# Optimization experiments

Measured on AMD Instinct MI355X. Metric: run time of the kernel, lower is better.

The kernel has to match this reference:

```python
import jax, jax.numpy as jnp
import numpy as np

D_MODEL = 1024
N_HEADS = 16
SCALES = (1, 2)
D_K = D_MODEL // N_HEADS          # 64
HPS = N_HEADS // len(SCALES)      # heads per scale = 8


def _upsample_linear(x, target_len):
    """PyTorch F.interpolate(mode='linear', align_corners=False) along dim 2.
    x: [b, h, l, d] -> [b, h, target_len, d]"""
    b, h, l, d = x.shape
    if l == target_len:
        return x
    # source coordinates, clamped at 0 like PyTorch's area_pixel_compute_source_index
    coords = (jnp.arange(target_len, dtype=jnp.float32) + 0.5) * (l / target_len) - 0.5
    coords = jnp.maximum(coords, 0.0)
    i0 = jnp.clip(jnp.floor(coords).astype(jnp.int32), 0, l - 1)
    i1 = jnp.minimum(i0 + 1, l - 1)
    w = (coords - i0.astype(jnp.float32))[None, None, :, None]
    return x[:, :, i0, :] * (1.0 - w) + x[:, :, i1, :] * w


def setup_inputs() -> dict:
    rng = jax.random.key(0)
    ks = jax.random.split(rng, 7)
    B, S = 2, 2048
    s = 1.0 / np.sqrt(D_MODEL)
    mkw = lambda k: jax.random.normal(k, (D_MODEL, D_MODEL), jnp.float32) * s
    zb = jnp.zeros((D_MODEL,), jnp.float32)
    return {
        "query": jax.random.normal(ks[0], (B, S, D_MODEL), jnp.float32),
        "key": jax.random.normal(ks[1], (B, S, D_MODEL), jnp.float32),
        "value": jax.random.normal(ks[2], (B, S, D_MODEL), jnp.float32),
        "w_q": mkw(ks[3]), "b_q": zb,
        "w_k": mkw(ks[4]), "b_k": zb,
        "w_v": mkw(ks[5]), "b_v": zb,
        "w_o": mkw(ks[6]), "b_o": zb,
    }


def reference(query, key, value, w_q, b_q, w_k, b_k, w_v, b_v, w_o, b_o):
    B, S, _ = query.shape
    inv_scale = 1.0 / np.sqrt(D_K).astype(np.float32)

    def proj(x, W, b):
        # [B,S,D] -> [B,H,S,dk]
        return (x @ W + b).reshape(B, S, N_HEADS, D_K).transpose(0, 2, 1, 3)

    Q = proj(query, w_q, b_q)
    K = proj(key, w_k, b_k)
    V = proj(value, w_v, b_v)

    outs = []
    for i, f in enumerate(SCALES):
        hs = slice(i * HPS, (i + 1) * HPS)
        Qd = Q[:, hs, ::f]                      # strided downsample along seq
        Kd = K[:, hs, ::f]
        Vd = V[:, hs, ::f]
        scores = jnp.einsum('bhqd,bhkd->bhqk', Qd, Kd) * inv_scale
        attn = jax.nn.softmax(scores, axis=-1)   # dropout inactive (eval)
        o = jnp.einsum('bhqk,bhkd->bhqd', attn, Vd)
        outs.append(_upsample_linear(o, S))

    out = jnp.concatenate(outs, axis=1)          # [B,H,S,dk]
    out = out.transpose(0, 2, 1, 3).reshape(B, S, D_MODEL)
    return out @ w_o + b_o
```

## Files before the change

kernel.cpp:

```cpp
#include <hip/hip_runtime.h>
#include <hip/hip_bf16.h>
#include <cstddef>

#define DMODEL 1024
#define DK 64
#define S1 2048
#define S2 1024
#define NBATCH 2
#define NSPLIT 2
#define KVTILE 64

typedef __bf16 bf16x8 __attribute__((ext_vector_type(8)));
typedef float f32x4 __attribute__((ext_vector_type(4)));
typedef unsigned short u16x4 __attribute__((ext_vector_type(4)));
typedef unsigned int u32x4 __attribute__((ext_vector_type(4)));

__device__ __forceinline__ unsigned short f2bf(float f) {
  unsigned u = __builtin_bit_cast(unsigned, f);
  u = (u + 0x7FFFu + ((u >> 16) & 1u)) >> 16;
  return (unsigned short)u;
}
__device__ __forceinline__ float bf2f(unsigned short u) {
  unsigned x = ((unsigned)u) << 16;
  return __builtin_bit_cast(float, x);
}
__device__ __forceinline__ unsigned pack2bf(float a, float b) {
  return (unsigned)f2bf(a) | ((unsigned)f2bf(b) << 16);
}
__device__ __forceinline__ bf16x8 ld_bf16x8(const unsigned short* p) {
  u32x4 v = *reinterpret_cast<const u32x4*>(p);
  return __builtin_bit_cast(bf16x8, v);
}
__device__ __forceinline__ void gload_lds16(const void* g, void* l) {
  __builtin_amdgcn_global_load_lds(
      (const __attribute__((address_space(1))) unsigned*)g,
      (__attribute__((address_space(3))) unsigned*)l, 16, 0, 0);
}
__device__ __forceinline__ bf16x8 ld_tile(const unsigned short* tile, int row, int cbytes) {
  const char* p = (const char*)tile + row * 128 + (cbytes ^ ((row & 7) << 4));
  return ld_bf16x8((const unsigned short*)p);
}

__global__ __launch_bounds__(256) void cvt_bf16_kernel(
    const float* __restrict__ in, unsigned short* __restrict__ out, int n4) {
  int i = blockIdx.x * 256 + threadIdx.x;
  if (i >= n4) return;
  f32x4 v = reinterpret_cast<const f32x4*>(in)[i];
  u16x4 r;
#pragma unroll
  for (int j = 0; j < 4; ++j) r[j] = f2bf(v[j]);
  reinterpret_cast<u16x4*>(out)[i] = r;
}

__global__ __launch_bounds__(1024) void transpose_w_kernel(
    const float* __restrict__ W, unsigned short* __restrict__ Wt) {
  __shared__ float t[32][33];
  int tx = threadIdx.x, ty = threadIdx.y;
  int n = blockIdx.x * 32 + tx;
  int k = blockIdx.y * 32 + ty;
  t[ty][tx] = W[(size_t)k * DMODEL + n];
  __syncthreads();
  int n2 = blockIdx.x * 32 + ty;
  int k2 = blockIdx.y * 32 + tx;
  Wt[(size_t)n2 * DMODEL + k2] = f2bf(t[tx][ty]);
}

template <int MODE>
__global__ __launch_bounds__(256) void gemm_bf16(
    const unsigned short* __restrict__ A, const unsigned short* __restrict__ Bt,
    const float* __restrict__ bias, float* __restrict__ outF,
    unsigned short* __restrict__ out1, unsigned short* __restrict__ out2) {
  __shared__ __align__(16) unsigned short As[2][128 * 64];
  __shared__ __align__(16) unsigned short Bs[2][64 * 64];
  int w = threadIdx.x >> 6, lane = threadIdx.x & 63;
  int lo = lane & 15, hi = lane >> 4;
  int rowBase = blockIdx.y * 128;
  int colBase = blockIdx.x * 64;
  int rl = lane >> 3;
  int ck = lane & 7;

  auto stageA = [&](int buf, int k0) {
#pragma unroll
    for (int i = 0; i < 4; ++i) {
      int slot = w * 4 + i;
      int rloc = slot * 8 + rl;
      int cb = (ck * 16) ^ ((rloc & 7) << 4);
      const char* g = (const char*)(A + (size_t)(rowBase + rloc) * DMODEL + k0) + cb;
      gload_lds16(g, (void*)&As[buf][slot * 512]);
    }
  };
  auto stageB = [&](int buf, int k0) {
#pragma unroll
    for (int i = 0; i < 2; ++i) {
      int slot = w * 2 + i;
      int rloc = slot * 8 + rl;
      int cb = (ck * 16) ^ ((rloc & 7) << 4);
      const char* g = (const char*)(Bt + (size_t)(colBase + rloc) * DMODEL + k0) + cb;
      gload_lds16(g, (void*)&Bs[buf][slot * 512]);
    }
  };

  f32x4 acc[2][4] = {};

  stageA(0, 0);
  stageB(0, 0);
  __syncthreads();

  const int NT = DMODEL / 64;
  for (int t = 0; t < NT; ++t) {
    int buf = t & 1;
    if (t + 1 < NT) {
      stageA(buf ^ 1, (t + 1) * 64);
      stageB(buf ^ 1, (t + 1) * 64);
    }
    bf16x8 af[2][2], bfr[4][2];
#pragma unroll
    for (int mt = 0; mt < 2; ++mt)
#pragma unroll
      for (int kk = 0; kk < 2; ++kk)
        af[mt][kk] = ld_tile(&As[buf][0], w * 32 + mt * 16 + lo, kk * 64 + hi * 16);
#pragma unroll
    for (int nt = 0; nt < 4; ++nt)
#pragma unroll
      for (int kk = 0; kk < 2; ++kk)
        bfr[nt][kk] = ld_tile(&Bs[buf][0], nt * 16 + lo, kk * 64 + hi * 16);
#pragma unroll
    for (int kk = 0; kk < 2; ++kk)
#pragma unroll
      for (int mt = 0; mt < 2; ++mt)
#pragma unroll
        for (int nt = 0; nt < 4; ++nt)
          acc[mt][nt] = __builtin_amdgcn_mfma_f32_16x16x32_bf16(
              af[mt][kk], bfr[nt][kk], acc[mt][nt], 0, 0, 0);
    __syncthreads();
  }

#pragma unroll
  for (int mt = 0; mt < 2; ++mt) {
#pragma unroll
    for (int nt = 0; nt < 4; ++nt) {
      int col = colBase + nt * 16 + lo;
      float bv = bias[col];
#pragma unroll
      for (int r = 0; r < 4; ++r) {
        int row = rowBase + w * 32 + mt * 16 + hi * 4 + r;
        float v = acc[mt][nt][r] + bv;
        if (MODE == 0) {
          outF[(size_t)row * DMODEL + col] = v;
        } else {
          int b = row >> 11, s = row & 2047;
          int h = col >> 6, d = col & 63;
          if (MODE == 1) {
            if (h < 8)
              out1[(((size_t)(b * 8 + h)) * S1 + s) * DK + d] = f2bf(v);
            else if (!(s & 1))
              out2[(((size_t)(b * 8 + (h - 8))) * S2 + (s >> 1)) * DK + d] = f2bf(v);
          } else {
            if (h < 8)
              out1[(((size_t)(b * 8 + h)) * DK + d) * S1 + s] = f2bf(v);
            else if (!(s & 1))
              out2[(((size_t)(b * 8 + (h - 8))) * DK + d) * S2 + (s >> 1)] = f2bf(v);
          }
        }
      }
    }
  }
}

__global__ __launch_bounds__(256) void attn_kernel(
    const unsigned short* __restrict__ Q, const unsigned short* __restrict__ K,
    const unsigned short* __restrict__ Vt, float* __restrict__ Opart,
    float* __restrict__ ml, int Sq, int Skv) {
  __shared__ __align__(16) unsigned short KV[2][2][64 * 64];
  __shared__ __align__(16) unsigned P_lds[4][16][36];
  int w = threadIdx.x >> 6, lane = threadIdx.x & 63;
  int lo = lane & 15, hi = lane >> 4;
  int bh = blockIdx.z;
  int split = blockIdx.y;
  int q0 = blockIdx.x * 64 + w * 16;
  int splitLen = Skv / NSPLIT;
  int kvbase = split * splitLen;
  int nIter = splitLen / KVTILE;

  const unsigned short* Qp = Q + ((size_t)bh * Sq + q0) * DK;
  bf16x8 qb0 = ld_bf16x8(Qp + lo * DK + hi * 8);
  bf16x8 qb1 = ld_bf16x8(Qp + lo * DK + 32 + hi * 8);

  const unsigned short* Kb = K + (size_t)bh * Skv * DK;
  const unsigned short* Vb = Vt + (size_t)bh * DK * Skv;

  auto stage = [&](int buf, int kv0) {
    int rl = lane >> 3;
    int cbl = (lane & 7) * 16;
#pragma unroll
    for (int i = 0; i < 2; ++i) {
      int rt = w * 16 + i * 8 + rl;
      int gcb = cbl ^ ((rt & 7) << 4);
      const char* gK = (const char*)(Kb + (size_t)(kv0 + rt) * DK) + gcb;
      gload_lds16(gK, (void*)&KV[buf][0][(w * 16 + i * 8) * 64]);
      const char* gV = (const char*)(Vb + (size_t)rt * Skv + kv0) + gcb;
      gload_lds16(gV, (void*)&KV[buf][1][(w * 16 + i * 8) * 64]);
    }
  };

  float m = -1e30f, l = 0.f;
  f32x4 oacc[4] = {};

  stage(0, kvbase);
  __syncthreads();

  for (int it = 0; it < nIter; ++it) {
    if (it + 1 < nIter) stage((it + 1) & 1, kvbase + (it + 1) * KVTILE);

    const unsigned short* Kt = &KV[it & 1][0][0];
    const unsigned short* Vtl = &KV[it & 1][1][0];

    f32x4 s[4];
#pragma unroll
    for (int t = 0; t < 4; ++t) {
      bf16x8 ka0 = ld_tile(Kt, t * 16 + lo, hi * 16);
      bf16x8 ka1 = ld_tile(Kt, t * 16 + lo, 64 + hi * 16);
      f32x4 z = {};
      z = __builtin_amdgcn_mfma_f32_16x16x32_bf16(ka0, qb0, z, 0, 0, 0);
      s[t] = __builtin_amdgcn_mfma_f32_16x16x32_bf16(ka1, qb1, z, 0, 0, 0);
    }

    float x[16];
#pragma unroll
    for (int t = 0; t < 4; ++t)
#pragma unroll
      for (int r = 0; r < 4; ++r) x[t * 4 + r] = s[t][r] * 0.125f;
    float tmax = x[0];
#pragma unroll
    for (int j = 1; j < 16; ++j) tmax = fmaxf(tmax, x[j]);
    tmax = fmaxf(tmax, __shfl_xor(tmax, 16));
    tmax = fmaxf(tmax, __shfl_xor(tmax, 32));
    float mnew = fmaxf(m, tmax);
    float alpha = __expf(m - mnew);
    m = mnew;
    float tsum = 0.f;
#pragma unroll
    for (int j = 0; j < 16; ++j) {
      x[j] = __expf(x[j] - mnew);
      tsum += x[j];
    }
    tsum += __shfl_xor(tsum, 16);
    tsum += __shfl_xor(tsum, 32);
    l = l * alpha + tsum;

    unsigned* prow = &P_lds[w][lo][0];
#pragma unroll
    for (int t = 0; t < 4; ++t) {
      uint2 pk;
      pk.x = pack2bf(x[t * 4 + 0], x[t * 4 + 1]);
      pk.y = pack2bf(x[t * 4 + 2], x[t * 4 + 3]);
      *reinterpret_cast<uint2*>(prow + t * 8 + 2 * hi) = pk;
    }

    float ar[4];
#pragma unroll
    for (int r = 0; r < 4; ++r) ar[r] = __shfl(alpha, hi * 4 + r);
#pragma unroll
    for (int nb = 0; nb < 4; ++nb) {
      f32x4 t = oacc[nb];
      t[0] *= ar[0];
      t[1] *= ar[1];
      t[2] *= ar[2];
      t[3] *= ar[3];
      oacc[nb] = t;
    }

    bf16x8 pa0 = ld_bf16x8(reinterpret_cast<unsigned short*>(prow + 4 * hi));
    bf16x8 pa1 = ld_bf16x8(reinterpret_cast<unsigned short*>(prow + 16 + 4 * hi));
#pragma unroll
    for (int nb = 0; nb < 4; ++nb) {
      bf16x8 vb0 = ld_tile(Vtl, nb * 16 + lo, hi * 16);
      bf16x8 vb1 = ld_tile(Vtl, nb * 16 + lo, 64 + hi * 16);
      oacc[nb] = __builtin_amdgcn_mfma_f32_16x16x32_bf16(pa0, vb0, oacc[nb], 0, 0, 0);
      oacc[nb] = __builtin_amdgcn_mfma_f32_16x16x32_bf16(pa1, vb1, oacc[nb], 0, 0, 0);
    }

    __syncthreads();
  }

  float* Op = Opart + (((size_t)(split * 16 + bh)) * Sq + q0) * DK;
#pragma unroll
  for (int nb = 0; nb < 4; ++nb)
#pragma unroll
    for (int r = 0; r < 4; ++r)
      Op[(size_t)(hi * 4 + r) * DK + nb * 16 + lo] = oacc[nb][r];
  if (hi == 0) {
    float2* mlp = reinterpret_cast<float2*>(ml) + ((size_t)(split * 16 + bh)) * Sq + q0 + lo;
    *mlp = make_float2(m, l);
  }
}

template <int MODE>
__global__ __launch_bounds__(256) void combine_kernel(
    const float* __restrict__ Opart, const float* __restrict__ ml,
    unsigned short* __restrict__ out, int Sq) {
  int rr = blockIdx.x * 4 + (threadIdx.x >> 6);
  int d = threadIdx.x & 63;
  int bh = rr / Sq, q = rr - bh * Sq;
  const float2* mlp = reinterpret_cast<const float2*>(ml);
  float2 ml0 = mlp[(size_t)bh * Sq + q];
  float2 ml1 = mlp[(size_t)(16 + bh) * Sq + q];
  float M = fmaxf(ml0.x, ml1.x);
  float w0 = __expf(ml0.x - M), w1 = __expf(ml1.x - M);
  float inv = 1.0f / (ml0.y * w0 + ml1.y * w1);
  float o0 = Opart[((size_t)bh * Sq + q) * DK + d];
  float o1 = Opart[((size_t)(16 + bh) * Sq + q) * DK + d];
  float v = (o0 * w0 + o1 * w1) * inv;
  if (MODE == 1) {
    int b = bh >> 3, h = bh & 7;
    out[((size_t)(b * S1 + q)) * DMODEL + h * 64 + d] = f2bf(v);
  } else {
    out[((size_t)bh * Sq + q) * DK + d] = f2bf(v);
  }
}

__global__ __launch_bounds__(256) void upsample_kernel(
    const unsigned short* __restrict__ O2, unsigned short* __restrict__ ctx) {
  int c = blockIdx.x * 256 + threadIdx.x;
  if (c >= NBATCH * S1 * 512) return;
  int col = c & 511;
  int m_ = c >> 9;
  int s = m_ & (S1 - 1);
  int b = m_ >> 11;
  int h = col >> 6, d = col & 63;
  const unsigned short* X = O2 + ((size_t)(b * 8 + h)) * S2 * DK + d;
  int mm = s >> 1;
  float v;
  if (s & 1) {
    int i1 = (mm + 1 < S2) ? mm + 1 : S2 - 1;
    v = 0.75f * bf2f(X[(size_t)mm * DK]) + 0.25f * bf2f(X[(size_t)i1 * DK]);
  } else {
    v = (mm == 0) ? bf2f(X[0])
                  : (0.25f * bf2f(X[(size_t)(mm - 1) * DK]) +
                     0.75f * bf2f(X[(size_t)mm * DK]));
  }
  ctx[((size_t)(b * S1 + s)) * DMODEL + 512 + col] = f2bf(v);
}

extern "C" void kernel_launch(void* const* d_in, const int* in_sizes, int n_in,
                              void* d_out, int out_size, void* d_ws, size_t ws_size,
                              hipStream_t stream) {
  const float* query = (const float*)d_in[0];
  const float* key = (const float*)d_in[1];
  const float* value = (const float*)d_in[2];
  const float* w_q = (const float*)d_in[3];
  const float* b_q = (const float*)d_in[4];
  const float* w_k = (const float*)d_in[5];
  const float* b_k = (const float*)d_in[6];
  const float* w_v = (const float*)d_in[7];
  const float* b_v = (const float*)d_in[8];
  const float* w_o = (const float*)d_in[9];
  const float* b_o = (const float*)d_in[10];
  float* out = (float*)d_out;

  char* ws = (char*)d_ws;
  size_t off = 0;
  auto alloc = [&](size_t bytes) {
    char* p = ws + off;
    off += (bytes + 255) & ~(size_t)255;
    return p;
  };
  const size_t WT_B = (size_t)DMODEL * DMODEL * 2;
  unsigned short* WqT = (unsigned short*)alloc(WT_B);
  unsigned short* WkT = (unsigned short*)alloc(WT_B);
  unsigned short* WvT = (unsigned short*)alloc(WT_B);
  unsigned short* WoT = (unsigned short*)alloc(WT_B);
  unsigned short* xk = (unsigned short*)alloc((size_t)NBATCH * S1 * DMODEL * 2);
  unsigned short* xv = (unsigned short*)alloc((size_t)NBATCH * S1 * DMODEL * 2);
  float* Opart1 = (float*)xk;
  unsigned short* Q1 = (unsigned short*)alloc((size_t)16 * S1 * DK * 2);
  unsigned short* K1 = (unsigned short*)alloc((size_t)16 * S1 * DK * 2);
  unsigned short* V1t = (unsigned short*)alloc((size_t)16 * S1 * DK * 2);
  unsigned short* Q2 = (unsigned short*)alloc((size_t)16 * S2 * DK * 2);
  unsigned short* K2 = (unsigned short*)alloc((size_t)16 * S2 * DK * 2);
  unsigned short* V2t = (unsigned short*)alloc((size_t)16 * S2 * DK * 2);
  unsigned short* O2 = (unsigned short*)alloc((size_t)16 * S2 * DK * 2);
  unsigned short* ctx = (unsigned short*)alloc((size_t)NBATCH * S1 * DMODEL * 2);
  unsigned short* xq = ctx;
  float* Opart2 = (float*)alloc((size_t)NSPLIT * 16 * S2 * DK * 4);
  float* ml1 = (float*)alloc((size_t)NSPLIT * 16 * S1 * 2 * 4);
  float* ml2 = (float*)alloc((size_t)NSPLIT * 16 * S2 * 2 * 4);

  const int n4 = NBATCH * S1 * DMODEL / 4;
  cvt_bf16_kernel<<<n4 / 256, 256, 0, stream>>>(query, xq, n4);
  cvt_bf16_kernel<<<n4 / 256, 256, 0, stream>>>(key, xk, n4);
  cvt_bf16_kernel<<<n4 / 256, 256, 0, stream>>>(value, xv, n4);

  dim3 tb(32, 32), tg(32, 32);
  transpose_w_kernel<<<tg, tb, 0, stream>>>(w_q, WqT);
  transpose_w_kernel<<<tg, tb, 0, stream>>>(w_k, WkT);
  transpose_w_kernel<<<tg, tb, 0, stream>>>(w_v, WvT);
  transpose_w_kernel<<<tg, tb, 0, stream>>>(w_o, WoT);

  dim3 gg(DMODEL / 64, (NBATCH * S1) / 128);
  gemm_bf16<1><<<gg, 256, 0, stream>>>(xq, WqT, b_q, nullptr, Q1, Q2);
  gemm_bf16<1><<<gg, 256, 0, stream>>>(xk, WkT, b_k, nullptr, K1, K2);
  gemm_bf16<2><<<gg, 256, 0, stream>>>(xv, WvT, b_v, nullptr, V1t, V2t);

  attn_kernel<<<dim3(S1 / 64, NSPLIT, 16), 256, 0, stream>>>(Q1, K1, V1t, Opart1, ml1, S1, S1);
  attn_kernel<<<dim3(S2 / 64, NSPLIT, 16), 256, 0, stream>>>(Q2, K2, V2t, Opart2, ml2, S2, S2);

  combine_kernel<1><<<(16 * S1) / 4, 256, 0, stream>>>(Opart1, ml1, ctx, S1);
  combine_kernel<0><<<(16 * S2) / 4, 256, 0, stream>>>(Opart2, ml2, O2, S2);

  upsample_kernel<<<(NBATCH * S1 * 512) / 256, 256, 0, stream>>>(O2, ctx);

  gemm_bf16<0><<<gg, 256, 0, stream>>>(ctx, WoT, b_o, out, nullptr, nullptr);
}
```

Baseline: 300.6 us.

## Fold softmax scale into Q projection, use exp2 and lazy rescaling

Multiplies Q in the projection epilogue by log2(e)/sqrt(dk) so the attention loop can drop its per-score scale and use exp2f in place of __expf. The online softmax now rescales the running max and the output accumulator only when some lane's tile max exceeds the stored max by more than 8, which skips the per-tile alpha shuffles and multiplies in the common case. The packed bf16 conversion becomes a single v_cvt_pk_bf16_f32 instruction. Rounding of Q to bf16 after scaling changes precision slightly, and exponentials of up to 2^8 before rescaling are accepted in exchange.

```diff
diff --git a/kernel.cpp b/kernel.cpp
--- a/kernel.cpp
+++ b/kernel.cpp
@@ -9,6 +9,7 @@
 #define NBATCH 2
 #define NSPLIT 2
 #define KVTILE 64
+#define QSCALE 0.1803368801111244f
 
 typedef __bf16 bf16x8 __attribute__((ext_vector_type(8)));
 typedef float f32x4 __attribute__((ext_vector_type(4)));
@@ -24,8 +25,10 @@
   unsigned x = ((unsigned)u) << 16;
   return __builtin_bit_cast(float, x);
 }
-__device__ __forceinline__ unsigned pack2bf(float a, float b) {
-  return (unsigned)f2bf(a) | ((unsigned)f2bf(b) << 16);
+__device__ __forceinline__ unsigned cvt_pk_bf16(float a, float b) {
+  unsigned r;
+  asm("v_cvt_pk_bf16_f32 %0, %1, %2" : "=v"(r) : "v"(a), "v"(b));
+  return r;
 }
 __device__ __forceinline__ bf16x8 ld_bf16x8(const unsigned short* p) {
   u32x4 v = *reinterpret_cast<const u32x4*>(p);
@@ -68,7 +71,7 @@
 template <int MODE>
 __global__ __launch_bounds__(256) void gemm_bf16(
     const unsigned short* __restrict__ A, const unsigned short* __restrict__ Bt,
-    const float* __restrict__ bias, float* __restrict__ outF,
+    const float* __restrict__ bias, float sc, float* __restrict__ outF,
     unsigned short* __restrict__ out1, unsigned short* __restrict__ out2) {
   __shared__ __align__(16) unsigned short As[2][128 * 64];
   __shared__ __align__(16) unsigned short Bs[2][64 * 64];
@@ -144,7 +147,7 @@
 #pragma unroll
       for (int r = 0; r < 4; ++r) {
         int row = rowBase + w * 32 + mt * 16 + hi * 4 + r;
-        float v = acc[mt][nt][r] + bv;
+        float v = (acc[mt][nt][r] + bv) * sc;
         if (MODE == 0) {
           outF[(size_t)row * DMODEL + col] = v;
         } else {
@@ -229,45 +232,49 @@
 #pragma unroll
     for (int t = 0; t < 4; ++t)
 #pragma unroll
-      for (int r = 0; r < 4; ++r) x[t * 4 + r] = s[t][r] * 0.125f;
+      for (int r = 0; r < 4; ++r) x[t * 4 + r] = s[t][r];
     float tmax = x[0];
 #pragma unroll
     for (int j = 1; j < 16; ++j) tmax = fmaxf(tmax, x[j]);
     tmax = fmaxf(tmax, __shfl_xor(tmax, 16));
     tmax = fmaxf(tmax, __shfl_xor(tmax, 32));
-    float mnew = fmaxf(m, tmax);
-    float alpha = __expf(m - mnew);
-    m = mnew;
+
+    if (!__all(tmax - m <= 8.0f)) {
+      float mnew = fmaxf(m, tmax);
+      float alpha = exp2f(m - mnew);
+      m = mnew;
+      l *= alpha;
+      float ar[4];
+#pragma unroll
+      for (int r = 0; r < 4; ++r) ar[r] = __shfl(alpha, hi * 4 + r);
+#pragma unroll
+      for (int nb = 0; nb < 4; ++nb) {
+        f32x4 t = oacc[nb];
+        t[0] *= ar[0];
+        t[1] *= ar[1];
+        t[2] *= ar[2];
+        t[3] *= ar[3];
+        oacc[nb] = t;
+      }
+    }
+
     float tsum = 0.f;
 #pragma unroll
     for (int j = 0; j < 16; ++j) {
-      x[j] = __expf(x[j] - mnew);
+      x[j] = exp2f(x[j] - m);
       tsum += x[j];
     }
     tsum += __shfl_xor(tsum, 16);
     tsum += __shfl_xor(tsum, 32);
-    l = l * alpha + tsum;
+    l += tsum;
 
     unsigned* prow = &P_lds[w][lo][0];
 #pragma unroll
     for (int t = 0; t < 4; ++t) {
       uint2 pk;
-      pk.x = pack2bf(x[t * 4 + 0], x[t * 4 + 1]);
-      pk.y = pack2bf(x[t * 4 + 2], x[t * 4 + 3]);
+      pk.x = cvt_pk_bf16(x[t * 4 + 0], x[t * 4 + 1]);
+      pk.y = cvt_pk_bf16(x[t * 4 + 2], x[t * 4 + 3]);
       *reinterpret_cast<uint2*>(prow + t * 8 + 2 * hi) = pk;
-    }
-
-    float ar[4];
-#pragma unroll
-    for (int r = 0; r < 4; ++r) ar[r] = __shfl(alpha, hi * 4 + r);
-#pragma unroll
-    for (int nb = 0; nb < 4; ++nb) {
-      f32x4 t = oacc[nb];
-      t[0] *= ar[0];
-      t[1] *= ar[1];
-      t[2] *= ar[2];
-      t[3] *= ar[3];
-      oacc[nb] = t;
     }
 
     bf16x8 pa0 = ld_bf16x8(reinterpret_cast<unsigned short*>(prow + 4 * hi));
@@ -306,7 +313,7 @@
   float2 ml0 = mlp[(size_t)bh * Sq + q];
   float2 ml1 = mlp[(size_t)(16 + bh) * Sq + q];
   float M = fmaxf(ml0.x, ml1.x);
-  float w0 = __expf(ml0.x - M), w1 = __expf(ml1.x - M);
+  float w0 = exp2f(ml0.x - M), w1 = exp2f(ml1.x - M);
   float inv = 1.0f / (ml0.y * w0 + ml1.y * w1);
   float o0 = Opart[((size_t)bh * Sq + q) * DK + d];
   float o1 = Opart[((size_t)(16 + bh) * Sq + q) * DK + d];
@@ -398,9 +405,9 @@
   transpose_w_kernel<<<tg, tb, 0, stream>>>(w_o, WoT);
 
   dim3 gg(DMODEL / 64, (NBATCH * S1) / 128);
-  gemm_bf16<1><<<gg, 256, 0, stream>>>(xq, WqT, b_q, nullptr, Q1, Q2);
-  gemm_bf16<1><<<gg, 256, 0, stream>>>(xk, WkT, b_k, nullptr, K1, K2);
-  gemm_bf16<2><<<gg, 256, 0, stream>>>(xv, WvT, b_v, nullptr, V1t, V2t);
+  gemm_bf16<1><<<gg, 256, 0, stream>>>(xq, WqT, b_q, QSCALE, nullptr, Q1, Q2);
+  gemm_bf16<1><<<gg, 256, 0, stream>>>(xk, WkT, b_k, 1.0f, nullptr, K1, K2);
+  gemm_bf16<2><<<gg, 256, 0, stream>>>(xv, WvT, b_v, 1.0f, nullptr, V1t, V2t);
 
   attn_kernel<<<dim3(S1 / 64, NSPLIT, 16), 256, 0, stream>>>(Q1, K1, V1t, Opart1, ml1, S1, S1);
   attn_kernel<<<dim3(S2 / 64, NSPLIT, 16), 256, 0, stream>>>(Q2, K2, V2t, Opart2, ml2, S2, S2);
@@ -410,5 +417,5 @@
 
   upsample_kernel<<<(NBATCH * S1 * 512) / 256, 256, 0, stream>>>(O2, ctx);
 
-  gemm_bf16<0><<<gg, 256, 0, stream>>>(ctx, WoT, b_o, out, nullptr, nullptr);
-}
+  gemm_bf16<0><<<gg, 256, 0, stream>>>(ctx, WoT, b_o, 1.0f, out, nullptr, nullptr);
+}
```

New measurement: 298.5 us. No clear change (-0.7%).
